# Optimization experiments

Hardware: AMD Instinct MI355X
Metric: run time of the kernel (lower is better)

The kernel has to match this reference:

```python
import jax, jax.numpy as jnp
import numpy as np

N = 100_000        # nodes
F_IN = 1024        # input features
H1, C1 = 8, 8      # layer-1 heads, per-head channels (concat -> 64)
C_OUT = 40         # num classes (layer-2, heads=1, concat=False)
E = 3_200_000      # directed edges (avg degree 32)
NEG_SLOPE = 0.2    # PyG GATConv default leaky_relu slope


def setup_inputs() -> dict:
    key = jax.random.key(0)
    ks = jax.random.split(key, 10)
    x = jax.random.normal(ks[0], (N, F_IN), jnp.float32)
    edge_index = jax.random.randint(ks[1], (2, E), 0, N, dtype=jnp.int32)
    s1 = 1.0 / np.sqrt(F_IN)
    W1 = jax.random.normal(ks[2], (F_IN, H1 * C1), jnp.float32) * s1
    sa = 1.0 / np.sqrt(C1)
    att_src1 = jax.random.normal(ks[3], (H1, C1), jnp.float32) * sa
    att_dst1 = jax.random.normal(ks[4], (H1, C1), jnp.float32) * sa
    b1 = jnp.zeros((H1 * C1,), jnp.float32)
    s2 = 1.0 / np.sqrt(H1 * C1)
    W2 = jax.random.normal(ks[5], (H1 * C1, C_OUT), jnp.float32) * s2
    so = 1.0 / np.sqrt(C_OUT)
    att_src2 = jax.random.normal(ks[6], (1, C_OUT), jnp.float32) * so
    att_dst2 = jax.random.normal(ks[7], (1, C_OUT), jnp.float32) * so
    b2 = jnp.zeros((C_OUT,), jnp.float32)
    return {"x": x, "edge_index": edge_index, "W1": W1, "att_src1": att_src1,
            "att_dst1": att_dst1, "b1": b1, "W2": W2, "att_src2": att_src2,
            "att_dst2": att_dst2, "b2": b2}


def gat_layer(x, src, dst, W, a_src, a_dst, b, heads, ch, concat, n):
    # per-head linear projection: [n, heads, ch]
    xw = (x @ W).reshape(n, heads, ch)
    # per-node attention logits: [n, heads]
    al_src = jnp.einsum('nhc,hc->nh', xw, a_src)
    al_dst = jnp.einsum('nhc,hc->nh', xw, a_dst)
    # per-edge scores (message src -> dst): [e, heads]
    e = jax.nn.leaky_relu(al_src[src] + al_dst[dst], NEG_SLOPE)
    # segment softmax over incoming edges of each dst node
    m = jax.ops.segment_max(e, dst, num_segments=n)          # [n, heads]
    p = jnp.exp(e - m[dst])
    denom = jax.ops.segment_sum(p, dst, num_segments=n)      # [n, heads]
    alpha = p / (denom[dst] + 1e-16)                          # [e, heads]
    # weighted scatter-sum of source features
    out = jax.ops.segment_sum(xw[src] * alpha[:, :, None], dst, num_segments=n)
    out = out.reshape(n, heads * ch) if concat else out.mean(axis=1)
    return out + b


def reference(x, edge_index, W1, att_src1, att_dst1, b1, W2, att_src2, att_dst2, b2):
    n = x.shape[0]
    # PyG GATConv default: add self loops
    loop = jnp.arange(n, dtype=edge_index.dtype)
    src = jnp.concatenate([edge_index[0], loop])
    dst = jnp.concatenate([edge_index[1], loop])
    h = jax.nn.elu(gat_layer(x, src, dst, W1, att_src1, att_dst1, b1, H1, C1, True, n))
    h = gat_layer(h, src, dst, W2, att_src2, att_dst2, b2, 1, C_OUT, False, n)
    return jax.nn.log_softmax(h, axis=1)
```

## Files before the change

kernel.cpp:

```cpp
#include <hip/hip_runtime.h>
#include <hip/hip_bf16.h>
#include <cstdint>
#include <cstddef>

#define F_IN 1024
#define F1 64
#define H1 8
#define C1 8
#define C_OUT 40
#define NEG 0.2f
#define LOG2E 1.442695040888963387f
#define B1 256
#define BSHIFT 9
#define BNODES 512

typedef __attribute__((ext_vector_type(8))) short short8;
typedef __attribute__((ext_vector_type(4))) float f32x4;

static __device__ __forceinline__ unsigned short f2bf(float f) {
  union { float f; unsigned u; } v; v.f = f;
  unsigned r = v.u + 0x7fff + ((v.u >> 16) & 1);
  return (unsigned short)(r >> 16);
}
static __device__ __forceinline__ float bf2f(unsigned short h) {
  union { unsigned u; float f; } v; v.u = ((unsigned)h) << 16; return v.f;
}
static __device__ __forceinline__ unsigned pkbf(float a, float b) {
  union { __hip_bfloat162 h; unsigned u; } c;
  c.h = __float22bfloat162_rn(float2{a, b});
  return c.u;
}
static __device__ __forceinline__ int rfl(int v) {
  return __builtin_amdgcn_readfirstlane(v);
}

__global__ __launch_bounds__(256) void w1cvt_kernel(const float* __restrict__ W1,
                                                    unsigned short* __restrict__ w1t) {
  int i = blockIdx.x * 256 + threadIdx.x;
  int c = i >> 10, k = i & 1023;
  w1t[i] = f2bf(W1[(size_t)k * F1 + c]);
}

__global__ __launch_bounds__(256) void gemm1_mfma(const float* __restrict__ x,
                                                  const unsigned short* __restrict__ w1t,
                                                  unsigned short* __restrict__ xw1, int n) {
  const int tid = threadIdx.x;
  const int wv = tid >> 6;
  const int l = tid & 63;
  const int lr = l & 15;
  const int lg = l >> 4;
  const int rowBase = blockIdx.x * 64 + wv * 16;
  int row = rowBase + lr;
  int rowc = row < n ? row : (n - 1);
  const float* px = x + (size_t)rowc * F_IN + lg * 8;

  f32x4 acc0 = {0.f, 0.f, 0.f, 0.f}, acc1 = acc0, acc2 = acc0, acc3 = acc0;

#pragma unroll 4
  for (int k0 = 0; k0 < F_IN; k0 += 32) {
    float4 xa = *(const float4*)(px + k0);
    float4 xb = *(const float4*)(px + k0 + 4);
    union { short8 s; unsigned u[4]; } af;
    af.u[0] = pkbf(xa.x, xa.y);
    af.u[1] = pkbf(xa.z, xa.w);
    af.u[2] = pkbf(xb.x, xb.y);
    af.u[3] = pkbf(xb.z, xb.w);
    const size_t kOff = (size_t)(k0 + lg * 8);
    short8 b0 = *(const short8*)(w1t + (size_t)(0 * 16 + lr) * F_IN + kOff);
    short8 b1 = *(const short8*)(w1t + (size_t)(1 * 16 + lr) * F_IN + kOff);
    short8 b2 = *(const short8*)(w1t + (size_t)(2 * 16 + lr) * F_IN + kOff);
    short8 b3 = *(const short8*)(w1t + (size_t)(3 * 16 + lr) * F_IN + kOff);
    acc0 = __builtin_amdgcn_mfma_f32_16x16x32_bf16(af.s, b0, acc0, 0, 0, 0);
    acc1 = __builtin_amdgcn_mfma_f32_16x16x32_bf16(af.s, b1, acc1, 0, 0, 0);
    acc2 = __builtin_amdgcn_mfma_f32_16x16x32_bf16(af.s, b2, acc2, 0, 0, 0);
    acc3 = __builtin_amdgcn_mfma_f32_16x16x32_bf16(af.s, b3, acc3, 0, 0, 0);
  }

#pragma unroll
  for (int r = 0; r < 4; ++r) {
    int orow = rowBase + lg * 4 + r;
    if (orow < n) {
      unsigned short* po = xw1 + (size_t)orow * F1 + lr;
      po[0]  = f2bf(acc0[r]);
      po[16] = f2bf(acc1[r]);
      po[32] = f2bf(acc2[r]);
      po[48] = f2bf(acc3[r]);
    }
  }
}

__global__ __launch_bounds__(256) void al1_kernel(const unsigned short* __restrict__ xw1,
    const float* __restrict__ asrc, const float* __restrict__ adst,
    float* __restrict__ al_src, float* __restrict__ al_dst, int n) {
  int id = blockIdx.x * 256 + threadIdx.x;
  if (id >= n * H1) return;
  int node = id >> 3, h = id & 7;
  const unsigned short* row = xw1 + (size_t)node * F1 + h * C1;
  float s = 0.f, d = 0.f;
#pragma unroll
  for (int c = 0; c < C1; ++c) {
    float v = bf2f(row[c]);
    s += v * asrc[h * C1 + c];
    d += v * adst[h * C1 + c];
  }
  al_src[id] = s * LOG2E;
  al_dst[id] = d * LOG2E;
}

__global__ __launch_bounds__(256) void binhist_kernel(const int* __restrict__ dst,
    int* __restrict__ cnt, int e, int nbuck) {
  __shared__ int lh[256];
  int tid = threadIdx.x, blk = blockIdx.x;
  lh[tid] = 0;
  __syncthreads();
  int chunk = (e + gridDim.x - 1) / gridDim.x;
  int s = blk * chunk, en = min(e, s + chunk);
  for (int i = s + tid; i < en; i += 256) atomicAdd(&lh[dst[i] >> BSHIFT], 1);
  __syncthreads();
  if (tid < nbuck) cnt[tid * B1 + blk] = lh[tid];
}

__global__ __launch_bounds__(256) void scan1_kernel(const int* __restrict__ in,
    int* __restrict__ excl, int* __restrict__ bsum, int len) {
  __shared__ int s[256];
  int tid = threadIdx.x;
  int gid = blockIdx.x * 256 + tid;
  int v = gid < len ? in[gid] : 0;
  s[tid] = v;
  __syncthreads();
  for (int ofs = 1; ofs < 256; ofs <<= 1) {
    int t = (tid >= ofs) ? s[tid - ofs] : 0;
    __syncthreads();
    s[tid] += t;
    __syncthreads();
  }
  if (gid < len) excl[gid] = s[tid] - v;
  if (tid == 255) bsum[blockIdx.x] = s[255];
}

__global__ __launch_bounds__(1024) void scan2_kernel(int* __restrict__ bsum, int nb) {
  __shared__ int s[1024];
  int tid = threadIdx.x;
  int v = tid < nb ? bsum[tid] : 0;
  s[tid] = v;
  __syncthreads();
  for (int ofs = 1; ofs < 1024; ofs <<= 1) {
    int t = (tid >= ofs) ? s[tid - ofs] : 0;
    __syncthreads();
    s[tid] += t;
    __syncthreads();
  }
  if (tid < nb) bsum[tid] = s[tid] - v;
}


__global__ __launch_bounds__(256) void binscatter_kernel(const int* __restrict__ src,
    const int* __restrict__ dst, const int* __restrict__ cntS,
    const int* __restrict__ bsum, unsigned* __restrict__ binned, int e, int nbuck) {
  __shared__ int lcur[256];
  int tid = threadIdx.x, blk = blockIdx.x;
  if (tid < nbuck) lcur[tid] = cntS[tid * B1 + blk] + bsum[tid];
  __syncthreads();
  int chunk = (e + gridDim.x - 1) / gridDim.x;
  int s = blk * chunk, en = min(e, s + chunk);
  for (int i = s + tid; i < en; i += 256) {
    int d = dst[i];
    int pos = atomicAdd(&lcur[d >> BSHIFT], 1);
    binned[pos] = ((unsigned)(d & (BNODES - 1)) << 23) | (unsigned)src[i];
  }
}

__global__ __launch_bounds__(256) void bucket_csr_kernel(const unsigned* __restrict__ binned,
    const int* __restrict__ bsum, int* __restrict__ deg, int* __restrict__ off,
    int* __restrict__ csr, int e, int n, int nbuck) {
  int q = blockIdx.x, tid = threadIdx.x;
  int eBase = bsum[q];
  int eEnd = (q + 1 < nbuck) ? bsum[q + 1] : e;
  __shared__ int nh[BNODES], sc[BNODES], cu[BNODES];
  nh[tid] = 0; nh[tid + 256] = 0;
  __syncthreads();
  for (int i = eBase + tid; i < eEnd; i += 256) atomicAdd(&nh[binned[i] >> 23], 1);
  __syncthreads();
  sc[tid] = nh[tid]; sc[tid + 256] = nh[tid + 256];
  __syncthreads();
  for (int ofs = 1; ofs < BNODES; ofs <<= 1) {
    int a0 = sc[tid], a1 = sc[tid + 256];
    int b0 = (tid >= ofs) ? sc[tid - ofs] : 0;
    int b1 = (tid + 256 >= ofs) ? sc[tid + 256 - ofs] : 0;
    __syncthreads();
    sc[tid] = a0 + b0; sc[tid + 256] = a1 + b1;
    __syncthreads();
  }
  int e0 = sc[tid] - nh[tid], e1 = sc[tid + 256] - nh[tid + 256];
  cu[tid] = e0; cu[tid + 256] = e1;
  int node0 = q * BNODES + tid, node1 = node0 + 256;
  if (node0 < n) { deg[node0] = nh[tid];       off[node0] = eBase + e0; }
  if (node1 < n) { deg[node1] = nh[tid + 256]; off[node1] = eBase + e1; }
  __syncthreads();
  for (int i = eBase + tid; i < eEnd; i += 256) {
    unsigned v = binned[i];
    int pos = eBase + atomicAdd(&cu[v >> 23], 1);
    csr[pos] = (int)(v & 0x7FFFFF);
  }
}

__global__ __launch_bounds__(256) void gat1_agg(const unsigned short* __restrict__ xw1,
    const float* __restrict__ al_src, const float* __restrict__ al_dst,
    const int* __restrict__ csr, const int* __restrict__ off, const int* __restrict__ deg,
    const float* __restrict__ b1, float* __restrict__ h1, int n) {
  const int node = rfl((int)((blockIdx.x * blockDim.x + threadIdx.x) >> 6));
  if (node >= n) return;
  const int lane = threadIdx.x & 63;
  const int half = lane >> 5;
  const int c2 = lane & 31;
  const int h = c2 >> 2;
  const int base = rfl(off[node]);
  const int cnt  = rfl(deg[node]);
  const float adst = al_dst[node * H1 + h];
  const int* __restrict__ csrp = csr + base;
  const char* xwB = (const char*)xw1;
  const char* alB = (const char*)al_src;
  const int cOff = c2 << 2;
  const int hOff = h << 2;

  float acc0 = 0.f, acc1 = 0.f, l = 0.f;

#define PAIR_BODY(wv_, av_) { \
    float t = (av_) + adst; \
    float sc = fmaxf(t, NEG * t); \
    float p = __builtin_amdgcn_exp2f(sc); \
    acc0 = fmaf(p, bf2f((unsigned short)((wv_) & 0xffffu)), acc0); \
    acc1 = fmaf(p, bf2f((unsigned short)((wv_) >> 16)), acc1); \
    l += p; }

  int it = 0;
  for (; it + 8 <= cnt; it += 8) {
    int xo[4];
#pragma unroll
    for (int jp = 0; jp < 4; ++jp) {
      int s0 = rfl(csrp[it + 2 * jp]) << 7;
      int s1 = rfl(csrp[it + 2 * jp + 1]) << 7;
      xo[jp] = half ? s1 : s0;
    }
    unsigned wv[4]; float av[4];
#pragma unroll
    for (int jp = 0; jp < 4; ++jp) {
      wv[jp] = *(const unsigned*)(xwB + xo[jp] + cOff);
      av[jp] = *(const float*)(alB + (xo[jp] >> 2) + hOff);
    }
#pragma unroll
    for (int jp = 0; jp < 4; ++jp) PAIR_BODY(wv[jp], av[jp]);
  }
  for (; it + 2 <= cnt; it += 2) {
    int s0 = rfl(csrp[it]) << 7;
    int s1 = rfl(csrp[it + 1]) << 7;
    int bs = half ? s1 : s0;
    unsigned w = *(const unsigned*)(xwB + bs + cOff);
    float av = *(const float*)(alB + (bs >> 2) + hOff);
    PAIR_BODY(w, av);
  }
  {
    const bool odd = (it < cnt);
    int sA = odd ? rfl(csrp[it]) : node;
    int bs = (half ? node : sA) << 7;
    unsigned w = *(const unsigned*)(xwB + bs + cOff);
    float av = *(const float*)(alB + (bs >> 2) + hOff);
    float t = av + adst;
    float sc = fmaxf(t, NEG * t);
    float p = __builtin_amdgcn_exp2f(sc);
    if (!odd && half) p = 0.f;
    acc0 = fmaf(p, bf2f((unsigned short)(w & 0xffffu)), acc0);
    acc1 = fmaf(p, bf2f((unsigned short)(w >> 16)), acc1);
    l += p;
  }
#undef PAIR_BODY

  acc0 += __shfl_xor(acc0, 32);
  acc1 += __shfl_xor(acc1, 32);
  l    += __shfl_xor(l, 32);
  if (half == 0) {
    float inv = 1.f / (l + 1e-16f);
    float2 bv = *(const float2*)(b1 + (c2 << 1));
    float o0 = acc0 * inv + bv.x;
    float o1 = acc1 * inv + bv.y;
    o0 = o0 > 0.f ? o0 : __expf(o0) - 1.f;
    o1 = o1 > 0.f ? o1 : __expf(o1) - 1.f;
    *(float2*)(h1 + (size_t)node * F1 + (c2 << 1)) = make_float2(o0, o1);
  }
}

__global__ __launch_bounds__(256) void gemm2_kernel(const float* __restrict__ h1,
    const float* __restrict__ W2, const float* __restrict__ asrc,
    const float* __restrict__ adst, unsigned short* __restrict__ xw2,
    float* __restrict__ alS2, float* __restrict__ alD2, int n) {
  __shared__ float ws[F1 * C_OUT];
  __shared__ float wsa[C_OUT], wsd[C_OUT];
  int tid = threadIdx.x;
  for (int i = tid; i < F1 * C_OUT; i += 256) ws[i] = W2[i];
  if (tid < C_OUT) { wsa[tid] = asrc[tid]; wsd[tid] = adst[tid]; }
  __syncthreads();
  int node = blockIdx.x * 256 + tid;
  if (node >= n) return;
  const float4* row4 = (const float4*)(h1 + (size_t)node * F1);
  float acc[C_OUT];
#pragma unroll
  for (int j = 0; j < C_OUT; ++j) acc[j] = 0.f;
#pragma unroll 2
  for (int k4 = 0; k4 < 16; ++k4) {
    float4 xv = row4[k4];
    const float* w0 = &ws[(4 * k4 + 0) * C_OUT];
    const float* w1 = &ws[(4 * k4 + 1) * C_OUT];
    const float* w2 = &ws[(4 * k4 + 2) * C_OUT];
    const float* w3 = &ws[(4 * k4 + 3) * C_OUT];
#pragma unroll
    for (int j = 0; j < C_OUT; j += 4) {
      float4 v0 = *(const float4*)(w0 + j);
      float4 v1 = *(const float4*)(w1 + j);
      float4 v2 = *(const float4*)(w2 + j);
      float4 v3 = *(const float4*)(w3 + j);
      acc[j + 0] += xv.x * v0.x + xv.y * v1.x + xv.z * v2.x + xv.w * v3.x;
      acc[j + 1] += xv.x * v0.y + xv.y * v1.y + xv.z * v2.y + xv.w * v3.y;
      acc[j + 2] += xv.x * v0.z + xv.y * v1.z + xv.z * v2.z + xv.w * v3.z;
      acc[j + 3] += xv.x * v0.w + xv.y * v1.w + xv.z * v2.w + xv.w * v3.w;
    }
  }
  float s = 0.f, d = 0.f;
#pragma unroll
  for (int j = 0; j < C_OUT; ++j) { s += acc[j] * wsa[j]; d += acc[j] * wsd[j]; }
  alS2[node] = s * LOG2E;
  alD2[node] = d * LOG2E;
  unsigned short* orow = xw2 + (size_t)node * C_OUT;
#pragma unroll
  for (int j = 0; j < C_OUT; j += 4) {
    ushort4 o;
    o.x = f2bf(acc[j + 0]); o.y = f2bf(acc[j + 1]);
    o.z = f2bf(acc[j + 2]); o.w = f2bf(acc[j + 3]);
    *(ushort4*)(orow + j) = o;
  }
}

__global__ __launch_bounds__(256) void gat2_agg(const unsigned short* __restrict__ xw2,
    const float* __restrict__ alS, const float* __restrict__ alD,
    const int* __restrict__ csr, const int* __restrict__ off, const int* __restrict__ deg,
    const float* __restrict__ b2, float* __restrict__ out, int n) {
  const int node = rfl((int)((blockIdx.x * blockDim.x + threadIdx.x) >> 6));
  if (node >= n) return;
  const int lane = threadIdx.x & 63;
  const int half = lane >> 5;
  const int c2 = lane & 31;
  const bool act = c2 < 20;
  const int c2r = act ? c2 : 0;
  const int base = rfl(off[node]);
  const int cnt  = rfl(deg[node]);
  const float adst = alD[node];
  const int* __restrict__ csrp = csr + base;
  const char* xwB = (const char*)xw2;
  const char* alB = (const char*)alS;
  const int cOff = c2r << 2;

  float acc0 = 0.f, acc1 = 0.f, l = 0.f;

#define PAIR_BODY2(wv_, av_) { \
    float t = (av_) + adst; \
    float sc = fmaxf(t, NEG * t); \
    float p = __builtin_amdgcn_exp2f(sc); \
    acc0 = fmaf(p, bf2f((unsigned short)((wv_) & 0xffffu)), acc0); \
    acc1 = fmaf(p, bf2f((unsigned short)((wv_) >> 16)), acc1); \
    l += p; }

  int it = 0;
  for (; it + 8 <= cnt; it += 8) {
    int xo[4], ao[4];
#pragma unroll
    for (int jp = 0; jp < 4; ++jp) {
      int s0 = rfl(csrp[it + 2 * jp]);
      int s1 = rfl(csrp[it + 2 * jp + 1]);
      xo[jp] = half ? s1 * 80 : s0 * 80;
      ao[jp] = half ? (s1 << 2) : (s0 << 2);
    }
    unsigned wv[4]; float av[4];
#pragma unroll
    for (int jp = 0; jp < 4; ++jp) {
      wv[jp] = *(const unsigned*)(xwB + xo[jp] + cOff);
      av[jp] = *(const float*)(alB + ao[jp]);
    }
#pragma unroll
    for (int jp = 0; jp < 4; ++jp) PAIR_BODY2(wv[jp], av[jp]);
  }
  for (; it + 2 <= cnt; it += 2) {
    int s0 = rfl(csrp[it]);
    int s1 = rfl(csrp[it + 1]);
    int bs = half ? s1 : s0;
    unsigned w = *(const unsigned*)(xwB + bs * 80 + cOff);
    float av = *(const float*)(alB + (bs << 2));
    PAIR_BODY2(w, av);
  }
  {
    const bool odd = (it < cnt);
    int sA = odd ? rfl(csrp[it]) : node;
    int bs = half ? node : sA;
    unsigned w = *(const unsigned*)(xwB + bs * 80 + cOff);
    float av = *(const float*)(alB + (bs << 2));
    float t = av + adst;
    float sc = fmaxf(t, NEG * t);
    float p = __builtin_amdgcn_exp2f(sc);
    if (!odd && half) p = 0.f;
    acc0 = fmaf(p, bf2f((unsigned short)(w & 0xffffu)), acc0);
    acc1 = fmaf(p, bf2f((unsigned short)(w >> 16)), acc1);
    l += p;
  }
#undef PAIR_BODY2

  acc0 += __shfl_xor(acc0, 32);
  acc1 += __shfl_xor(acc1, 32);
  l    += __shfl_xor(l, 32);

  float inv = 1.f / (l + 1e-16f);
  float v0 = -1e30f, v1 = -1e30f;
  if (act) {
    float2 bv = *(const float2*)(b2 + (c2 << 1));
    v0 = acc0 * inv + bv.x;
    v1 = acc1 * inv + bv.y;
  }
  float mx = fmaxf(v0, v1);
#pragma unroll
  for (int mask = 1; mask <= 16; mask <<= 1) mx = fmaxf(mx, __shfl_xor(mx, mask));
  float e0 = act ? __expf(v0 - mx) : 0.f;
  float e1 = act ? __expf(v1 - mx) : 0.f;
  float sum = e0 + e1;
#pragma unroll
  for (int mask = 1; mask <= 16; mask <<= 1) sum += __shfl_xor(sum, mask);
  if (half == 0 && act) {
    float ls = __logf(sum);
    *(float2*)(out + (size_t)node * C_OUT + (c2 << 1)) =
        make_float2(v0 - mx - ls, v1 - mx - ls);
  }
}

extern "C" void kernel_launch(void* const* d_in, const int* in_sizes, int n_in,
                              void* d_out, int out_size, void* d_ws, size_t ws_size,
                              hipStream_t stream) {
  const float* x   = (const float*)d_in[0];
  const int*   ei  = (const int*)d_in[1];
  const float* W1  = (const float*)d_in[2];
  const float* as1 = (const float*)d_in[3];
  const float* ad1 = (const float*)d_in[4];
  const float* b1  = (const float*)d_in[5];
  const float* W2  = (const float*)d_in[6];
  const float* as2 = (const float*)d_in[7];
  const float* ad2 = (const float*)d_in[8];
  const float* b2  = (const float*)d_in[9];
  float* out = (float*)d_out;

  const int n = in_sizes[0] / F_IN;
  const int e = in_sizes[1] / 2;
  const int* srcIdx = ei;
  const int* dstIdx = ei + e;
  const int nbuck = (n + BNODES - 1) >> BSHIFT;
  const int clen = nbuck * B1;

  char* p = (char*)d_ws;
  auto take = [&](size_t bytes) {
    char* q = p;
    p += (bytes + 255) & ~(size_t)255;
    return q;
  };
  unsigned short* xw1 = (unsigned short*)take((size_t)n * F1 * 2);
  float* h1           = (float*)take((size_t)n * F1 * 4);
  unsigned short* xw2 = (unsigned short*)take((size_t)n * C_OUT * 2);
  unsigned short* w1t = (unsigned short*)take((size_t)F_IN * F1 * 2);
  float* alS1 = (float*)take((size_t)n * H1 * 4);
  float* alD1 = (float*)take((size_t)n * H1 * 4);
  float* alS2 = (float*)take((size_t)n * 4);
  float* alD2 = (float*)take((size_t)n * 4);
  int* deg  = (int*)take((size_t)n * 4);
  int* offb = (int*)take((size_t)n * 4);
  int* cnt  = (int*)take((size_t)clen * 4);
  int* cntS = (int*)take((size_t)clen * 4);
  int* bsum = (int*)take(4096);
  unsigned* binned = (unsigned*)take((size_t)e * 4);
  int* csr  = (int*)take((size_t)e * 4);

  dim3 b256(256);
  w1cvt_kernel<<<dim3((F_IN * F1) / 256), b256, 0, stream>>>(W1, w1t);
  gemm1_mfma<<<dim3((n + 63) / 64), b256, 0, stream>>>(x, w1t, xw1, n);
  al1_kernel<<<dim3((n * H1 + 255) / 256), b256, 0, stream>>>(xw1, as1, ad1, alS1, alD1, n);

  binhist_kernel<<<dim3(B1), b256, 0, stream>>>(dstIdx, cnt, e, nbuck);
  int nbScan = (clen + 255) / 256;
  scan1_kernel<<<dim3(nbScan), b256, 0, stream>>>(cnt, cntS, bsum, clen);
  scan2_kernel<<<dim3(1), dim3(1024), 0, stream>>>(bsum, nbScan);
  binscatter_kernel<<<dim3(B1), b256, 0, stream>>>(srcIdx, dstIdx, cntS, bsum, binned, e, nbuck);
  bucket_csr_kernel<<<dim3(nbuck), b256, 0, stream>>>(binned, bsum, deg, offb, csr, e, n, nbuck);

  gat1_agg<<<dim3((n + 3) / 4), b256, 0, stream>>>(xw1, alS1, alD1, csr, offb, deg, b1, h1, n);
  gemm2_kernel<<<dim3((n + 255) / 256), b256, 0, stream>>>(h1, W2, as2, ad2, xw2, alS2, alD2, n);
  gat2_agg<<<dim3((n + 3) / 4), b256, 0, stream>>>(xw2, alS2, alD2, csr, offb, deg, b2, out, n);
}
```

Baseline: 470.5 us.

## Fuse CSR build phases with GEMM1 and attention-logit kernels via block-range dispatch

Merges the destination histogram into the GEMM1 launch with a block-index split, and fuses the bucket scan and per-node degree scan with the attention-logit kernel. Per-node degrees are now counted with global atomics during the histogram pass, so the per-bucket CSR kernel only scatters into precomputed offsets. Bucket placement uses a global atomic cursor instead of a full prefix scan over the count matrix. The goal is fewer launches and overlap of edge preprocessing with the dense GEMM. The cost is 3.2M global atomics on deg and an extra memset, and within-node edge order now depends on atomic timing, which can change floating-point summation order.

```diff
diff --git a/kernel.cpp b/kernel.cpp
--- a/kernel.cpp
+++ b/kernel.cpp
@@ -41,15 +41,36 @@
   w1t[i] = f2bf(W1[(size_t)k * F1 + c]);
 }
 
-__global__ __launch_bounds__(256) void gemm1_mfma(const float* __restrict__ x,
-                                                  const unsigned short* __restrict__ w1t,
-                                                  unsigned short* __restrict__ xw1, int n) {
+__global__ __launch_bounds__(256) void k1_hist_gemm(const float* __restrict__ x,
+    const unsigned short* __restrict__ w1t, unsigned short* __restrict__ xw1,
+    const int* __restrict__ dst, int* __restrict__ cnt, int* __restrict__ btot,
+    int* __restrict__ deg, int n, int e, int nbuck) {
+  const int bid = blockIdx.x;
   const int tid = threadIdx.x;
+  if (bid < B1) {
+    __shared__ int lh[256];
+    lh[tid] = 0;
+    __syncthreads();
+    int chunk = (e + B1 - 1) / B1;
+    int s = bid * chunk, en = min(e, s + chunk);
+    for (int i = s + tid; i < en; i += 256) {
+      int d = dst[i];
+      atomicAdd(&lh[d >> BSHIFT], 1);
+      atomicAdd(&deg[d], 1);
+    }
+    __syncthreads();
+    if (tid < nbuck) {
+      cnt[tid * B1 + bid] = lh[tid];
+      atomicAdd(&btot[tid], lh[tid]);
+    }
+    return;
+  }
+  const int gb = bid - B1;
   const int wv = tid >> 6;
   const int l = tid & 63;
   const int lr = l & 15;
   const int lg = l >> 4;
-  const int rowBase = blockIdx.x * 64 + wv * 16;
+  const int rowBase = gb * 64 + wv * 16;
   int row = rowBase + lr;
   int rowc = row < n ? row : (n - 1);
   const float* px = x + (size_t)rowc * F_IN + lg * 8;
@@ -89,10 +110,51 @@
   }
 }
 
-__global__ __launch_bounds__(256) void al1_kernel(const unsigned short* __restrict__ xw1,
-    const float* __restrict__ asrc, const float* __restrict__ adst,
-    float* __restrict__ al_src, float* __restrict__ al_dst, int n) {
-  int id = blockIdx.x * 256 + threadIdx.x;
+__global__ __launch_bounds__(256) void k2_scan_al1(const int* __restrict__ btot,
+    int* __restrict__ bstart, int* __restrict__ gcur,
+    const int* __restrict__ deg, int* __restrict__ off, int* __restrict__ bsumN,
+    const unsigned short* __restrict__ xw1, const float* __restrict__ asrc,
+    const float* __restrict__ adst, float* __restrict__ al_src,
+    float* __restrict__ al_dst, int n, int e, int nbuck, int nbScanN) {
+  const int bid = blockIdx.x;
+  const int tid = threadIdx.x;
+  if (bid == 0) {
+    __shared__ int s[256];
+    int v = tid < nbuck ? btot[tid] : 0;
+    s[tid] = v;
+    __syncthreads();
+    for (int ofs = 1; ofs < 256; ofs <<= 1) {
+      int t = (tid >= ofs) ? s[tid - ofs] : 0;
+      __syncthreads();
+      s[tid] += t;
+      __syncthreads();
+    }
+    if (tid < nbuck) {
+      int ex = s[tid] - v;
+      bstart[tid] = ex;
+      gcur[tid] = ex;
+    }
+    if (tid == nbuck - 1) bstart[nbuck] = s[tid];
+    return;
+  }
+  if (bid < 1 + nbScanN) {
+    __shared__ int s[256];
+    int sblk = bid - 1;
+    int gid = sblk * 256 + tid;
+    int v = gid < n ? deg[gid] : 0;
+    s[tid] = v;
+    __syncthreads();
+    for (int ofs = 1; ofs < 256; ofs <<= 1) {
+      int t = (tid >= ofs) ? s[tid - ofs] : 0;
+      __syncthreads();
+      s[tid] += t;
+      __syncthreads();
+    }
+    if (gid < n) off[gid] = s[tid] - v;
+    if (tid == 255) bsumN[sblk] = s[255];
+    return;
+  }
+  int id = (bid - 1 - nbScanN) * 256 + tid;
   if (id >= n * H1) return;
   int node = id >> 3, h = id & 7;
   const unsigned short* row = xw1 + (size_t)node * F1 + h * C1;
@@ -107,61 +169,35 @@
   al_dst[id] = d * LOG2E;
 }
 
-__global__ __launch_bounds__(256) void binhist_kernel(const int* __restrict__ dst,
-    int* __restrict__ cnt, int e, int nbuck) {
-  __shared__ int lh[256];
-  int tid = threadIdx.x, blk = blockIdx.x;
-  lh[tid] = 0;
+__global__ __launch_bounds__(256) void k3_scan_scatter(int* __restrict__ bsumN,
+    const int* __restrict__ src, const int* __restrict__ dst,
+    const int* __restrict__ cnt, int* __restrict__ gcur,
+    unsigned* __restrict__ binned, int e, int nbuck, int nbScanN) {
+  const int bid = blockIdx.x;
+  const int tid = threadIdx.x;
+  if (bid == 0) {
+    __shared__ int s[512];
+    int v0 = tid < nbScanN ? bsumN[tid] : 0;
+    int v1 = (tid + 256) < nbScanN ? bsumN[tid + 256] : 0;
+    s[tid] = v0; s[tid + 256] = v1;
+    __syncthreads();
+    for (int ofs = 1; ofs < 512; ofs <<= 1) {
+      int a0 = s[tid], a1 = s[tid + 256];
+      int b0 = (tid >= ofs) ? s[tid - ofs] : 0;
+      int b1 = (tid + 256 >= ofs) ? s[tid + 256 - ofs] : 0;
+      __syncthreads();
+      s[tid] = a0 + b0; s[tid + 256] = a1 + b1;
+      __syncthreads();
+    }
+    if (tid < nbScanN) bsumN[tid] = s[tid] - v0;
+    if (tid + 256 < nbScanN) bsumN[tid + 256] = s[tid + 256] - v1;
+    return;
+  }
+  __shared__ int lcur[256];
+  int blk = bid - 1;
+  if (tid < nbuck) lcur[tid] = atomicAdd(&gcur[tid], cnt[tid * B1 + blk]);
   __syncthreads();
-  int chunk = (e + gridDim.x - 1) / gridDim.x;
-  int s = blk * chunk, en = min(e, s + chunk);
-  for (int i = s + tid; i < en; i += 256) atomicAdd(&lh[dst[i] >> BSHIFT], 1);
-  __syncthreads();
-  if (tid < nbuck) cnt[tid * B1 + blk] = lh[tid];
-}
-
-__global__ __launch_bounds__(256) void scan1_kernel(const int* __restrict__ in,
-    int* __restrict__ excl, int* __restrict__ bsum, int len) {
-  __shared__ int s[256];
-  int tid = threadIdx.x;
-  int gid = blockIdx.x * 256 + tid;
-  int v = gid < len ? in[gid] : 0;
-  s[tid] = v;
-  __syncthreads();
-  for (int ofs = 1; ofs < 256; ofs <<= 1) {
-    int t = (tid >= ofs) ? s[tid - ofs] : 0;
-    __syncthreads();
-    s[tid] += t;
-    __syncthreads();
-  }
-  if (gid < len) excl[gid] = s[tid] - v;
-  if (tid == 255) bsum[blockIdx.x] = s[255];
-}
-
-__global__ __launch_bounds__(1024) void scan2_kernel(int* __restrict__ bsum, int nb) {
-  __shared__ int s[1024];
-  int tid = threadIdx.x;
-  int v = tid < nb ? bsum[tid] : 0;
-  s[tid] = v;
-  __syncthreads();
-  for (int ofs = 1; ofs < 1024; ofs <<= 1) {
-    int t = (tid >= ofs) ? s[tid - ofs] : 0;
-    __syncthreads();
-    s[tid] += t;
-    __syncthreads();
-  }
-  if (tid < nb) bsum[tid] = s[tid] - v;
-}
-
-
-__global__ __launch_bounds__(256) void binscatter_kernel(const int* __restrict__ src,
-    const int* __restrict__ dst, const int* __restrict__ cntS,
-    const int* __restrict__ bsum, unsigned* __restrict__ binned, int e, int nbuck) {
-  __shared__ int lcur[256];
-  int tid = threadIdx.x, blk = blockIdx.x;
-  if (tid < nbuck) lcur[tid] = cntS[tid * B1 + blk] + bsum[tid];
-  __syncthreads();
-  int chunk = (e + gridDim.x - 1) / gridDim.x;
+  int chunk = (e + B1 - 1) / B1;
   int s = blk * chunk, en = min(e, s + chunk);
   for (int i = s + tid; i < en; i += 256) {
     int d = dst[i];
@@ -170,36 +206,26 @@
   }
 }
 
-__global__ __launch_bounds__(256) void bucket_csr_kernel(const unsigned* __restrict__ binned,
-    const int* __restrict__ bsum, int* __restrict__ deg, int* __restrict__ off,
-    int* __restrict__ csr, int e, int n, int nbuck) {
+__global__ __launch_bounds__(256) void scan3_kernel(int* __restrict__ arr,
+    const int* __restrict__ bsumx, int len) {
+  int gid = blockIdx.x * 256 + threadIdx.x;
+  if (gid < len) arr[gid] += bsumx[blockIdx.x];
+}
+
+__global__ __launch_bounds__(256) void bucket_lite_kernel(const unsigned* __restrict__ binned,
+    const int* __restrict__ bstart, const int* __restrict__ off,
+    int* __restrict__ csr, int n, int nbuck) {
   int q = blockIdx.x, tid = threadIdx.x;
-  int eBase = bsum[q];
-  int eEnd = (q + 1 < nbuck) ? bsum[q + 1] : e;
-  __shared__ int nh[BNODES], sc[BNODES], cu[BNODES];
-  nh[tid] = 0; nh[tid + 256] = 0;
-  __syncthreads();
-  for (int i = eBase + tid; i < eEnd; i += 256) atomicAdd(&nh[binned[i] >> 23], 1);
-  __syncthreads();
-  sc[tid] = nh[tid]; sc[tid + 256] = nh[tid + 256];
-  __syncthreads();
-  for (int ofs = 1; ofs < BNODES; ofs <<= 1) {
-    int a0 = sc[tid], a1 = sc[tid + 256];
-    int b0 = (tid >= ofs) ? sc[tid - ofs] : 0;
-    int b1 = (tid + 256 >= ofs) ? sc[tid + 256 - ofs] : 0;
-    __syncthreads();
-    sc[tid] = a0 + b0; sc[tid + 256] = a1 + b1;
-    __syncthreads();
-  }
-  int e0 = sc[tid] - nh[tid], e1 = sc[tid + 256] - nh[tid + 256];
-  cu[tid] = e0; cu[tid + 256] = e1;
-  int node0 = q * BNODES + tid, node1 = node0 + 256;
-  if (node0 < n) { deg[node0] = nh[tid];       off[node0] = eBase + e0; }
-  if (node1 < n) { deg[node1] = nh[tid + 256]; off[node1] = eBase + e1; }
+  int eBase = bstart[q];
+  int eEnd = bstart[q + 1];
+  __shared__ int cu[BNODES];
+  int n0 = q * BNODES + tid, n1 = n0 + 256;
+  cu[tid] = n0 < n ? off[n0] : 0;
+  cu[tid + 256] = n1 < n ? off[n1] : 0;
   __syncthreads();
   for (int i = eBase + tid; i < eEnd; i += 256) {
     unsigned v = binned[i];
-    int pos = eBase + atomicAdd(&cu[v >> 23], 1);
+    int pos = atomicAdd(&cu[v >> 23], 1);
     csr[pos] = (int)(v & 0x7FFFFF);
   }
 }
@@ -215,7 +241,7 @@
   const int c2 = lane & 31;
   const int h = c2 >> 2;
   const int base = rfl(off[node]);
-  const int cnt  = rfl(deg[node]);
+  const int cnt = rfl(deg[node]);
   const float adst = al_dst[node * H1 + h];
   const int* __restrict__ csrp = csr + base;
   const char* xwB = (const char*)xw1;
@@ -351,7 +377,7 @@
   const bool act = c2 < 20;
   const int c2r = act ? c2 : 0;
   const int base = rfl(off[node]);
-  const int cnt  = rfl(deg[node]);
+  const int cnt = rfl(deg[node]);
   const float adst = alD[node];
   const int* __restrict__ csrp = csr + base;
   const char* xwB = (const char*)xw2;
@@ -457,7 +483,7 @@
   const int* srcIdx = ei;
   const int* dstIdx = ei + e;
   const int nbuck = (n + BNODES - 1) >> BSHIFT;
-  const int clen = nbuck * B1;
+  const int nbScanN = (n + 255) / 256;
 
   char* p = (char*)d_ws;
   auto take = [&](size_t bytes) {
@@ -473,25 +499,31 @@
   float* alD1 = (float*)take((size_t)n * H1 * 4);
   float* alS2 = (float*)take((size_t)n * 4);
   float* alD2 = (float*)take((size_t)n * 4);
-  int* deg  = (int*)take((size_t)n * 4);
-  int* offb = (int*)take((size_t)n * 4);
-  int* cnt  = (int*)take((size_t)clen * 4);
-  int* cntS = (int*)take((size_t)clen * 4);
-  int* bsum = (int*)take(4096);
+  int* deg    = (int*)take((size_t)n * 4);
+  int* btot   = (int*)take(256 * 4);
+  int* bstart = (int*)take(257 * 4);
+  int* gcur   = (int*)take(256 * 4);
+  int* offb   = (int*)take((size_t)n * 4);
+  int* cnt    = (int*)take((size_t)nbuck * B1 * 4);
+  int* bsumN  = (int*)take(2048);
   unsigned* binned = (unsigned*)take((size_t)e * 4);
-  int* csr  = (int*)take((size_t)e * 4);
+  int* csr    = (int*)take((size_t)e * 4);
+
+  hipMemsetAsync(deg, 0, (size_t)n * 4, stream);
+  hipMemsetAsync(btot, 0, 256 * 4, stream);
 
   dim3 b256(256);
+  const int gB = (n + 63) / 64;
   w1cvt_kernel<<<dim3((F_IN * F1) / 256), b256, 0, stream>>>(W1, w1t);
-  gemm1_mfma<<<dim3((n + 63) / 64), b256, 0, stream>>>(x, w1t, xw1, n);
-  al1_kernel<<<dim3((n * H1 + 255) / 256), b256, 0, stream>>>(xw1, as1, ad1, alS1, alD1, n);
-
-  binhist_kernel<<<dim3(B1), b256, 0, stream>>>(dstIdx, cnt, e, nbuck);
-  int nbScan = (clen + 255) / 256;
-  scan1_kernel<<<dim3(nbScan), b256, 0, stream>>>(cnt, cntS, bsum, clen);
-  scan2_kernel<<<dim3(1), dim3(1024), 0, stream>>>(bsum, nbScan);
-  binscatter_kernel<<<dim3(B1), b256, 0, stream>>>(srcIdx, dstIdx, cntS, bsum, binned, e, nbuck);
-  bucket_csr_kernel<<<dim3(nbuck), b256, 0, stream>>>(binned, bsum, deg, offb, csr, e, n, nbuck);
+  k1_hist_gemm<<<dim3(B1 + gB), b256, 0, stream>>>(x, w1t, xw1, dstIdx, cnt, btot,
+                                                   deg, n, e, nbuck);
+  const int alB = (n * H1 + 255) / 256;
+  k2_scan_al1<<<dim3(1 + nbScanN + alB), b256, 0, stream>>>(btot, bstart, gcur,
+      deg, offb, bsumN, xw1, as1, ad1, alS1, alD1, n, e, nbuck, nbScanN);
+  k3_scan_scatter<<<dim3(1 + B1), b256, 0, stream>>>(bsumN, srcIdx, dstIdx, cnt,
+      gcur, binned, e, nbuck, nbScanN);
+  scan3_kernel<<<dim3(nbScanN), b256, 0, stream>>>(offb, bsumN, n);
+  bucket_lite_kernel<<<dim3(nbuck), b256, 0, stream>>>(binned, bstart, offb, csr, n, nbuck);
 
   gat1_agg<<<dim3((n + 3) / 4), b256, 0, stream>>>(xw1, alS1, alD1, csr, offb, deg, b1, h1, n);
   gemm2_kernel<<<dim3((n + 255) / 256), b256, 0, stream>>>(h1, W2, as2, ad2, xw2, alS2, alD2, n);
```

Measured after the change: 523.1 us. +11.2%, slower.
